# Kernel tuning notes

Measured on AMD Instinct MI355X. Metric: run time of the kernel, lower is better.

## Reference

```python
import jax, jax.numpy as jnp
import numpy as np

B, DZ, L = 1, 128, 256
H, DC = 4, 32
DHC = H * DC


def setup_inputs() -> dict:
    key = jax.random.key(0)
    ks = jax.random.split(key, 6)
    s = 0.02
    return {
        "z": jax.random.normal(ks[0], (B, DZ, L, L), dtype=jnp.float32),
        "ln_w": jnp.ones((DZ,), jnp.float32),
        "ln_b": jnp.zeros((DZ,), jnp.float32),
        "wq": jax.random.normal(ks[1], (DZ, DHC), jnp.float32) * s,
        "bq": jnp.zeros((DHC,), jnp.float32),
        "wk": jax.random.normal(ks[2], (DZ, DHC), jnp.float32) * s,
        "bk": jnp.zeros((DHC,), jnp.float32),
        "wv": jax.random.normal(ks[3], (DZ, DHC), jnp.float32) * s,
        "bv": jnp.zeros((DHC,), jnp.float32),
        "wg": jax.random.normal(ks[4], (DZ, DHC), jnp.float32) * s,
        "bg": jnp.zeros((DHC,), jnp.float32),
        "w2": jax.random.normal(ks[5], (DHC, DZ), jnp.float32) * s,
        "b2": jnp.zeros((DZ,), jnp.float32),
    }


def reference(z, ln_w, ln_b, wq, bq, wk, bk, wv, bv, wg, bg, w2, b2):
    # z: (B, C, L, L) -> (B, n, i, dz)
    zp = jnp.transpose(z, (0, 2, 3, 1))
    # LayerNorm over last dim (torch eps=1e-5)
    mu = jnp.mean(zp, axis=-1, keepdims=True)
    var = jnp.mean(jnp.square(zp - mu), axis=-1, keepdims=True)
    zn = (zp - mu) * jax.lax.rsqrt(var + 1e-5) * ln_w + ln_b

    def proj(w, b):  # (B,n,i,dz) -> (B,n,i,H,DC)
        return (zn @ w + b).reshape(zn.shape[:-1] + (H, DC))

    scalar = jnp.sqrt(jnp.float32(1.0 / DC))
    q = proj(wq, bq)
    k = proj(wk, bk)
    v = proj(wv, bv)
    attn = jnp.einsum('bnihc,bnjhc->bhnij', q * scalar, k)
    attn_w = jax.nn.softmax(attn, axis=-1)
    o = jnp.einsum('bhnij,bnjhc->bnihc', attn_w, v)
    g = jax.nn.sigmoid(zn @ wg + bg).reshape(o.shape)
    zo = (o * g).reshape(o.shape[:-2] + (DHC,))
    out = (zo @ w2 + b2)
    return jnp.transpose(out, (0, 3, 1, 2))  # (B, C, L, L)
```

## Files before the change

### kernel.cpp

```cpp
#include <hip/hip_runtime.h>
#include <cstdint>
#include <cstddef>

#define DZc   128
#define Lc    256
#define Hc    4
#define DCc   32
#define DHCc  128
#define NPOSc (Lc * Lc)

typedef __attribute__((ext_vector_type(8))) short bf16x8;
typedef __attribute__((ext_vector_type(4))) short bf16x4;
typedef __attribute__((ext_vector_type(4))) float f32x4;

static __device__ __forceinline__ unsigned short f2bf(float f) {
  unsigned u = __float_as_uint(f);
  u += 0x7FFFu + ((u >> 16) & 1u);
  return (unsigned short)(u >> 16);
}
static __device__ __forceinline__ float bf2f(unsigned short h) {
  return __uint_as_float(((unsigned)h) << 16);
}
static __device__ __forceinline__ float sigmoidf_(float x) {
  return 1.0f / (1.0f + __expf(-x));
}
static __device__ __forceinline__ unsigned cvtpk(float lo, float hi) {
  unsigned r;
  asm("v_cvt_pk_bf16_f32 %0, %1, %2" : "=v"(r) : "v"(lo), "v"(hi));
  return r;
}

__global__ __launch_bounds__(256) void prep_weights(
    const float* __restrict__ wq, const float* __restrict__ wk,
    const float* __restrict__ wv, const float* __restrict__ wg,
    const float* __restrict__ w2, unsigned short* __restrict__ wT)
{
  const int b = blockIdx.x;
  const int t = threadIdx.x;
  const float* src = (b == 0) ? wq : (b == 1) ? wk : (b == 2) ? wv : (b == 3) ? wg : w2;
  unsigned short* dst = wT + (size_t)b * (DZc * DHCc);
  const float scale = (b == 0) ? 0.17677669529663687f : 1.0f;
  for (int p = 0; p < 64; ++p) {
    const int idx = p * 256 + t;
    const int kk = idx >> 7, j = idx & 127;
    dst[j * 128 + kk] = f2bf(src[idx] * scale);
  }
}

__global__ __launch_bounds__(512, 2) void fused_ln_proj_attn(
    const float* __restrict__ z, const float* __restrict__ lnw, const float* __restrict__ lnb,
    const unsigned short* __restrict__ wT,
    const float* __restrict__ bq, const float* __restrict__ bk,
    const float* __restrict__ bv, const float* __restrict__ bg,
    const float* __restrict__ b2, float* __restrict__ out)
{
  __shared__ unsigned short zkl[Lc * DZc];
  __shared__ unsigned short vtl[DHCc * Lc];
  __shared__ unsigned short pll[8][16 * 64];

  const int t  = threadIdx.x;
  const int n  = blockIdx.x;
  const int w8 = t >> 6;
  const int l  = t & 63;
  const int lr = l & 15;
  const int lg = l >> 4;
  const int h     = w8 & 3;
  const int ihalf = w8 >> 2;

  char* zkb = reinterpret_cast<char*>(zkl);
  char* vtb = reinterpret_cast<char*>(vtl);
  char* plb = reinterpret_cast<char*>(&pll[w8][0]);

  #pragma unroll
  for (int p = 0; p < 2; ++p) {
    const int pq = t >> 4;
    const int cg = t & 15;
    const int gp = n * 256 + p * 128 + pq * 4;
    const int cbase = cg * 8;

    float4 zr[8];
    #pragma unroll
    for (int cc = 0; cc < 8; ++cc)
      zr[cc] = *reinterpret_cast<const float4*>(&z[(size_t)(cbase + cc) * NPOSc + gp]);

    float s[4] = {0.f, 0.f, 0.f, 0.f}, s2[4] = {0.f, 0.f, 0.f, 0.f};
    #pragma unroll
    for (int cc = 0; cc < 8; ++cc) {
      s[0] += zr[cc].x; s2[0] += zr[cc].x * zr[cc].x;
      s[1] += zr[cc].y; s2[1] += zr[cc].y * zr[cc].y;
      s[2] += zr[cc].z; s2[2] += zr[cc].z * zr[cc].z;
      s[3] += zr[cc].w; s2[3] += zr[cc].w * zr[cc].w;
    }
    #pragma unroll
    for (int m = 1; m <= 8; m <<= 1) {
      #pragma unroll
      for (int e = 0; e < 4; ++e) {
        s[e]  += __shfl_xor(s[e],  m);
        s2[e] += __shfl_xor(s2[e], m);
      }
    }
    float mu[4], rs[4];
    #pragma unroll
    for (int e = 0; e < 4; ++e) {
      mu[e] = s[e] * (1.0f / DZc);
      const float var = s2[e] * (1.0f / DZc) - mu[e] * mu[e];
      rs[e] = rsqrtf(var + 1e-5f);
    }
    float lw[8], lb[8];
    #pragma unroll
    for (int q4 = 0; q4 < 2; ++q4) {
      const float4 a = *reinterpret_cast<const float4*>(&lnw[cbase + q4 * 4]);
      const float4 b = *reinterpret_cast<const float4*>(&lnb[cbase + q4 * 4]);
      lw[q4 * 4 + 0] = a.x; lw[q4 * 4 + 1] = a.y; lw[q4 * 4 + 2] = a.z; lw[q4 * 4 + 3] = a.w;
      lb[q4 * 4 + 0] = b.x; lb[q4 * 4 + 1] = b.y; lb[q4 * 4 + 2] = b.z; lb[q4 * 4 + 3] = b.w;
    }
    #pragma unroll
    for (int e = 0; e < 4; ++e) {
      const int i = p * 128 + pq * 4 + e;
      float zn[8];
      #pragma unroll
      for (int cc = 0; cc < 8; ++cc) {
        const float zc = (e == 0) ? zr[cc].x : (e == 1) ? zr[cc].y
                       : (e == 2) ? zr[cc].z : zr[cc].w;
        zn[cc] = (zc - mu[e]) * rs[e] * lw[cc] + lb[cc];
      }
      uint4 pw;
      pw.x = cvtpk(zn[0], zn[1]); pw.y = cvtpk(zn[2], zn[3]);
      pw.z = cvtpk(zn[4], zn[5]); pw.w = cvtpk(zn[6], zn[7]);
      int byte = i * 256 + cbase * 2;
      byte ^= ((i & 15) << 4);
      *reinterpret_cast<uint4*>(zkb + byte) = pw;
    }
  }
  __syncthreads();

  const unsigned short* wqT = wT;
  const unsigned short* wkT = wT + 1 * (DZc * DHCc);
  const unsigned short* wvT = wT + 2 * (DZc * DHCc);
  const unsigned short* wgT = wT + 3 * (DZc * DHCc);

  bf16x8 qfrag[8];
  {
    bf16x8 bfq[2][4];
    float4 qb4[2];
    #pragma unroll
    for (int jt = 0; jt < 2; ++jt) {
      #pragma unroll
      for (int kt = 0; kt < 4; ++kt)
        bfq[jt][kt] = *reinterpret_cast<const bf16x8*>(
            &wqT[(size_t)(h * 32 + jt * 16 + lr) * 128 + kt * 32 + lg * 8]);
      qb4[jt] = *reinterpret_cast<const float4*>(&bq[h * 32 + jt * 16 + lg * 4]);
      qb4[jt].x *= 0.17677669529663687f; qb4[jt].y *= 0.17677669529663687f;
      qb4[jt].z *= 0.17677669529663687f; qb4[jt].w *= 0.17677669529663687f;
    }
    #pragma unroll
    for (int it = 0; it < 8; ++it) {
      bf16x8 af[4];
      #pragma unroll
      for (int kt = 0; kt < 4; ++kt) {
        const int i = ihalf * 128 + it * 16 + lr;
        int byte = i * 256 + (kt * 64 + lg * 16);
        byte ^= ((i & 15) << 4);
        af[kt] = *reinterpret_cast<const bf16x8*>(zkb + byte);
      }
      f32x4 qa[2];
      qa[0] = (f32x4){0.f, 0.f, 0.f, 0.f};
      qa[1] = (f32x4){0.f, 0.f, 0.f, 0.f};
      #pragma unroll
      for (int kt = 0; kt < 4; ++kt)
        #pragma unroll
        for (int jt = 0; jt < 2; ++jt)
          qa[jt] = __builtin_amdgcn_mfma_f32_16x16x32_bf16(bfq[jt][kt], af[kt], qa[jt], 0, 0, 0);
      unsigned srcw0[2], srcw1[2];
      srcw0[0] = cvtpk(qa[0][0] + qb4[0].x, qa[0][1] + qb4[0].y);
      srcw0[1] = cvtpk(qa[0][2] + qb4[0].z, qa[0][3] + qb4[0].w);
      srcw1[0] = cvtpk(qa[1][0] + qb4[1].x, qa[1][1] + qb4[1].y);
      srcw1[1] = cvtpk(qa[1][2] + qb4[1].z, qa[1][3] + qb4[1].w);
      unsigned qw[4];
      #pragma unroll
      for (int i4 = 0; i4 < 4; ++i4) {
        const int quad = lg * 2 + (i4 >> 1);
        const int srcl = (quad & 3) * 16 + lr;
        const unsigned a = (unsigned)__shfl((int)srcw0[i4 & 1], srcl);
        const unsigned b = (unsigned)__shfl((int)srcw1[i4 & 1], srcl);
        qw[i4] = (lg >= 2) ? b : a;
      }
      uint4 qv; qv.x = qw[0]; qv.y = qw[1]; qv.z = qw[2]; qv.w = qw[3];
      qfrag[it] = *reinterpret_cast<const bf16x8*>(&qv);
    }
  }

  unsigned gpk[8][2][2];
  {
    bf16x8 bfg[2][4];
    float gb[2];
    #pragma unroll
    for (int jt = 0; jt < 2; ++jt) {
      #pragma unroll
      for (int kt = 0; kt < 4; ++kt)
        bfg[jt][kt] = *reinterpret_cast<const bf16x8*>(
            &wgT[(size_t)(h * 32 + jt * 16 + lr) * 128 + kt * 32 + lg * 8]);
      gb[jt] = bg[h * 32 + jt * 16 + lr];
    }
    #pragma unroll
    for (int it = 0; it < 8; ++it) {
      bf16x8 af[4];
      #pragma unroll
      for (int kt = 0; kt < 4; ++kt) {
        const int i = ihalf * 128 + it * 16 + lr;
        int byte = i * 256 + (kt * 64 + lg * 16);
        byte ^= ((i & 15) << 4);
        af[kt] = *reinterpret_cast<const bf16x8*>(zkb + byte);
      }
      f32x4 ga[2];
      ga[0] = (f32x4){0.f, 0.f, 0.f, 0.f};
      ga[1] = (f32x4){0.f, 0.f, 0.f, 0.f};
      #pragma unroll
      for (int kt = 0; kt < 4; ++kt)
        #pragma unroll
        for (int jt = 0; jt < 2; ++jt)
          ga[jt] = __builtin_amdgcn_mfma_f32_16x16x32_bf16(af[kt], bfg[jt][kt], ga[jt], 0, 0, 0);
      #pragma unroll
      for (int jt = 0; jt < 2; ++jt) {
        gpk[it][jt][0] = cvtpk(sigmoidf_(ga[jt][0] + gb[jt]), sigmoidf_(ga[jt][1] + gb[jt]));
        gpk[it][jt][1] = cvtpk(sigmoidf_(ga[jt][2] + gb[jt]), sigmoidf_(ga[jt][3] + gb[jt]));
      }
    }
  }

  {
    const int chq = w8 & 3, vih = w8 >> 2;
    bf16x8 bfv[2][4];
    float vb[2];
    #pragma unroll
    for (int jt = 0; jt < 2; ++jt) {
      #pragma unroll
      for (int kt = 0; kt < 4; ++kt)
        bfv[jt][kt] = *reinterpret_cast<const bf16x8*>(
            &wvT[(size_t)(chq * 32 + jt * 16 + lr) * 128 + kt * 32 + lg * 8]);
      vb[jt] = bv[chq * 32 + jt * 16 + lr];
    }
    #pragma unroll 1
    for (int it = 0; it < 8; ++it) {
      bf16x8 af[4];
      #pragma unroll
      for (int kt = 0; kt < 4; ++kt) {
        const int i = vih * 128 + it * 16 + lr;
        int byte = i * 256 + (kt * 64 + lg * 16);
        byte ^= ((i & 15) << 4);
        af[kt] = *reinterpret_cast<const bf16x8*>(zkb + byte);
      }
      f32x4 va[2];
      va[0] = (f32x4){0.f, 0.f, 0.f, 0.f};
      va[1] = (f32x4){0.f, 0.f, 0.f, 0.f};
      #pragma unroll
      for (int kt = 0; kt < 4; ++kt)
        #pragma unroll
        for (int jt = 0; jt < 2; ++jt)
          va[jt] = __builtin_amdgcn_mfma_f32_16x16x32_bf16(af[kt], bfv[jt][kt], va[jt], 0, 0, 0);
      const int ii0 = vih * 128 + it * 16 + lg * 4;
      #pragma unroll
      for (int jt = 0; jt < 2; ++jt) {
        const int ch = chq * 32 + jt * 16 + lr;
        uint2 pv;
        pv.x = cvtpk(va[jt][0] + vb[jt], va[jt][1] + vb[jt]);
        pv.y = cvtpk(va[jt][2] + vb[jt], va[jt][3] + vb[jt]);
        int byte = ch * 512 + ii0 * 2;
        byte ^= ((ch & 7) << 4);
        *reinterpret_cast<uint2*>(vtb + byte) = pv;
      }
    }
  }

  {
    bf16x8 bfk[4];
    #pragma unroll
    for (int kt = 0; kt < 4; ++kt)
      bfk[kt] = *reinterpret_cast<const bf16x8*>(
          &wkT[(size_t)(w8 * 16 + lr) * 128 + kt * 32 + lg * 8]);
    const float4 kb4 = *reinterpret_cast<const float4*>(&bk[w8 * 16 + lg * 4]);
    const float kb[4] = {kb4.x, kb4.y, kb4.z, kb4.w};

    #pragma unroll 1
    for (int c = 0; c < 4; ++c) {
      bf16x8 afr[4][4];
      #pragma unroll
      for (int itc = 0; itc < 4; ++itc)
        #pragma unroll
        for (int kt = 0; kt < 4; ++kt) {
          const int i = c * 64 + itc * 16 + lr;
          int byte = i * 256 + (kt * 64 + lg * 16);
          byte ^= ((i & 15) << 4);
          afr[itc][kt] = *reinterpret_cast<const bf16x8*>(zkb + byte);
        }
      __syncthreads();
      #pragma unroll
      for (int itc = 0; itc < 4; ++itc) {
        f32x4 ka = (f32x4){0.f, 0.f, 0.f, 0.f};
        #pragma unroll
        for (int kt = 0; kt < 4; ++kt)
          ka = __builtin_amdgcn_mfma_f32_16x16x32_bf16(bfk[kt], afr[itc][kt], ka, 0, 0, 0);
        const int j = c * 64 + itc * 16 + lr;
        uint2 pkk;
        pkk.x = cvtpk(ka[0] + kb[0], ka[1] + kb[1]);
        pkk.y = cvtpk(ka[2] + kb[2], ka[3] + kb[3]);
        int byte = j * 256 + (w8 * 16 + lg * 4) * 2;
        byte ^= ((j & 15) << 4);
        *reinterpret_cast<uint2*>(zkb + byte) = pkk;
      }
      __syncthreads();
    }
  }

  unsigned ogpk[8][4];
  #pragma unroll
  for (int it = 0; it < 8; ++it) {
    f32x4 sacc[16];
    #pragma unroll
    for (int jt = 0; jt < 16; ++jt) sacc[jt] = (f32x4){0.f, 0.f, 0.f, 0.f};
    #pragma unroll
    for (int jt = 0; jt < 16; ++jt) {
      const int j = jt * 16 + lr;
      int byte = j * 256 + h * 64 + lg * 16;
      byte ^= ((j & 15) << 4);
      bf16x8 kf = *reinterpret_cast<const bf16x8*>(zkb + byte);
      sacc[jt] = __builtin_amdgcn_mfma_f32_16x16x32_bf16(kf, qfrag[it], sacc[jt], 0, 0, 0);
    }

    float psum = 0.f;
    #pragma unroll
    for (int jt = 0; jt < 16; ++jt)
      #pragma unroll
      for (int r = 0; r < 4; ++r) {
        const float e = __expf(sacc[jt][r]);
        sacc[jt][r] = e;
        psum += e;
      }
    psum += __shfl_xor(psum, 16);
    psum += __shfl_xor(psum, 32);
    const float rl = 1.0f / psum;

    f32x4 oacc[2];
    oacc[0] = (f32x4){0.f, 0.f, 0.f, 0.f};
    oacc[1] = (f32x4){0.f, 0.f, 0.f, 0.f};
    #pragma unroll
    for (int qr = 0; qr < 4; ++qr) {
      #pragma unroll
      for (int jj = 0; jj < 4; ++jj) {
        const int jt = qr * 4 + jj;
        uint2 pk;
        pk.x = cvtpk(sacc[jt][0], sacc[jt][1]);
        pk.y = cvtpk(sacc[jt][2], sacc[jt][3]);
        int byte = lr * 128 + (jj * 16 + lg * 4) * 2;
        byte ^= ((lr & 7) << 4);
        *reinterpret_cast<uint2*>(plb + byte) = pk;
      }
      asm volatile("s_waitcnt lgkmcnt(0)" ::: "memory");
      __builtin_amdgcn_sched_barrier(0);
      #pragma unroll
      for (int kq = 0; kq < 2; ++kq) {
        int pbyte = lr * 128 + (kq * 64 + lg * 16);
        pbyte ^= ((lr & 7) << 4);
        bf16x8 pf = *reinterpret_cast<const bf16x8*>(plb + pbyte);
        #pragma unroll
        for (int cht = 0; cht < 2; ++cht) {
          const int ch = h * 32 + cht * 16 + lr;
          int vbyte = ch * 512 + (qr * 128 + kq * 64 + lg * 16);
          vbyte ^= ((ch & 7) << 4);
          bf16x8 vf = *reinterpret_cast<const bf16x8*>(vtb + vbyte);
          oacc[cht] = __builtin_amdgcn_mfma_f32_16x16x32_bf16(pf, vf, oacc[cht], 0, 0, 0);
        }
      }
    }

    {
      #pragma unroll
      for (int cht = 0; cht < 2; ++cht)
        #pragma unroll
        for (int rp = 0; rp < 2; ++rp) {
          const float g0 = bf2f((unsigned short)(gpk[it][cht][rp] & 0xffffu));
          const float g1 = bf2f((unsigned short)(gpk[it][cht][rp] >> 16));
          ogpk[it][cht * 2 + rp] = cvtpk(oacc[cht][rp * 2 + 0] * rl * g0,
                                         oacc[cht][rp * 2 + 1] * rl * g1);
        }
    }
  }

  __syncthreads();
  #pragma unroll
  for (int it = 0; it < 8; ++it)
    #pragma unroll
    for (int cht = 0; cht < 2; ++cht)
      #pragma unroll
      for (int r = 0; r < 4; ++r) {
        const int pos = ihalf * 128 + it * 16 + lg * 4 + r;
        const int ch  = h * 32 + cht * 16 + lr;
        int byte = pos * 256 + ch * 2;
        byte ^= ((pos & 15) << 4);
        *reinterpret_cast<unsigned short*>(zkb + byte) =
            (unsigned short)(ogpk[it][cht * 2 + (r >> 1)] >> ((r & 1) * 16));
      }
  __syncthreads();

  {
    const unsigned short* w2T = wT + 4 * (DZc * DHCc);
    bf16x8 zb[2][4];
    #pragma unroll
    for (int sub = 0; sub < 2; ++sub) {
      const int pos = w8 * 32 + sub * 16 + lr;
      #pragma unroll
      for (int kt = 0; kt < 4; ++kt) {
        int byte = pos * 256 + kt * 64 + lg * 16;
        byte ^= ((pos & 15) << 4);
        zb[sub][kt] = *reinterpret_cast<const bf16x8*>(zkb + byte);
      }
    }
    #pragma unroll
    for (int ct = 0; ct < 8; ++ct) {
      bf16x8 af[4];
      #pragma unroll
      for (int kt = 0; kt < 4; ++kt)
        af[kt] = *reinterpret_cast<const bf16x8*>(
            &w2T[(size_t)(ct * 16 + lr) * 128 + kt * 32 + lg * 8]);
      #pragma unroll
      for (int sub = 0; sub < 2; ++sub) {
        f32x4 acc = (f32x4){0.f, 0.f, 0.f, 0.f};
        #pragma unroll
        for (int kt = 0; kt < 4; ++kt)
          acc = __builtin_amdgcn_mfma_f32_16x16x32_bf16(af[kt], zb[sub][kt], acc, 0, 0, 0);
        const size_t gpos = (size_t)n * 256 + w8 * 32 + sub * 16 + lr;
        #pragma unroll
        for (int r = 0; r < 4; ++r) {
          const int c = ct * 16 + lg * 4 + r;
          out[(size_t)c * NPOSc + gpos] = acc[r] + b2[c];
        }
      }
    }
  }
}

extern "C" void kernel_launch(void* const* d_in, const int* in_sizes, int n_in,
                              void* d_out, int out_size, void* d_ws, size_t ws_size,
                              hipStream_t stream) {
  const float* z   = (const float*)d_in[0];
  const float* lnw = (const float*)d_in[1];
  const float* lnb = (const float*)d_in[2];
  const float* wq  = (const float*)d_in[3];
  const float* bq  = (const float*)d_in[4];
  const float* wk  = (const float*)d_in[5];
  const float* bk  = (const float*)d_in[6];
  const float* wv  = (const float*)d_in[7];
  const float* bv  = (const float*)d_in[8];
  const float* wg  = (const float*)d_in[9];
  const float* bg  = (const float*)d_in[10];
  const float* w2  = (const float*)d_in[11];
  const float* b2  = (const float*)d_in[12];
  float* out = (float*)d_out;

  unsigned short* wT = (unsigned short*)d_ws;

  prep_weights<<<5, 256, 0, stream>>>(wq, wk, wv, wg, w2, wT);
  fused_ln_proj_attn<<<Lc, 512, 0, stream>>>(
      z, lnw, lnb, wT, bq, bk, bv, bg, b2, out);
}
```

Baseline: 69.72 us.

## Chunk score computation per 64-key block and hoist K projection barriers

The attention loop now computes QK scores, exponentials and P·V for one 64-key chunk at a time, so only 4 score accumulators are live instead of 16. The softmax row sum is reduced after all chunks. The K projection is restructured to compute all 16 tiles into registers first, then write them back to LDS after a single barrier, replacing 8 barriers with 2. This aims to lower register pressure and synchronisation cost, but holds 16 uint2 K results in registers across the projection.

```diff
diff --git a/kernel.cpp b/kernel.cpp
--- a/kernel.cpp
+++ b/kernel.cpp
@@ -272,6 +272,7 @@
     }
   }
 
+  uint2 kreg[16];
   {
     bf16x8 bfk[4];
     #pragma unroll
@@ -281,76 +282,69 @@
     const float4 kb4 = *reinterpret_cast<const float4*>(&bk[w8 * 16 + lg * 4]);
     const float kb[4] = {kb4.x, kb4.y, kb4.z, kb4.w};
 
-    #pragma unroll 1
-    for (int c = 0; c < 4; ++c) {
-      bf16x8 afr[4][4];
-      #pragma unroll
-      for (int itc = 0; itc < 4; ++itc)
-        #pragma unroll
-        for (int kt = 0; kt < 4; ++kt) {
-          const int i = c * 64 + itc * 16 + lr;
-          int byte = i * 256 + (kt * 64 + lg * 16);
-          byte ^= ((i & 15) << 4);
-          afr[itc][kt] = *reinterpret_cast<const bf16x8*>(zkb + byte);
-        }
-      __syncthreads();
-      #pragma unroll
-      for (int itc = 0; itc < 4; ++itc) {
-        f32x4 ka = (f32x4){0.f, 0.f, 0.f, 0.f};
-        #pragma unroll
-        for (int kt = 0; kt < 4; ++kt)
-          ka = __builtin_amdgcn_mfma_f32_16x16x32_bf16(bfk[kt], afr[itc][kt], ka, 0, 0, 0);
-        const int j = c * 64 + itc * 16 + lr;
-        uint2 pkk;
-        pkk.x = cvtpk(ka[0] + kb[0], ka[1] + kb[1]);
-        pkk.y = cvtpk(ka[2] + kb[2], ka[3] + kb[3]);
-        int byte = j * 256 + (w8 * 16 + lg * 4) * 2;
-        byte ^= ((j & 15) << 4);
-        *reinterpret_cast<uint2*>(zkb + byte) = pkk;
-      }
-      __syncthreads();
-    }
-  }
+    #pragma unroll
+    for (int itt = 0; itt < 16; ++itt) {
+      bf16x8 af[4];
+      #pragma unroll
+      for (int kt = 0; kt < 4; ++kt) {
+        const int i = itt * 16 + lr;
+        int byte = i * 256 + (kt * 64 + lg * 16);
+        byte ^= ((i & 15) << 4);
+        af[kt] = *reinterpret_cast<const bf16x8*>(zkb + byte);
+      }
+      f32x4 ka = (f32x4){0.f, 0.f, 0.f, 0.f};
+      #pragma unroll
+      for (int kt = 0; kt < 4; ++kt)
+        ka = __builtin_amdgcn_mfma_f32_16x16x32_bf16(bfk[kt], af[kt], ka, 0, 0, 0);
+      kreg[itt].x = cvtpk(ka[0] + kb[0], ka[1] + kb[1]);
+      kreg[itt].y = cvtpk(ka[2] + kb[2], ka[3] + kb[3]);
+    }
+  }
+  __syncthreads();
+
+  #pragma unroll
+  for (int itt = 0; itt < 16; ++itt) {
+    const int j = itt * 16 + lr;
+    int byte = j * 256 + (w8 * 16 + lg * 4) * 2;
+    byte ^= ((j & 15) << 4);
+    *reinterpret_cast<uint2*>(zkb + byte) = kreg[itt];
+  }
+  __syncthreads();
 
   unsigned ogpk[8][4];
   #pragma unroll
   for (int it = 0; it < 8; ++it) {
-    f32x4 sacc[16];
-    #pragma unroll
-    for (int jt = 0; jt < 16; ++jt) sacc[jt] = (f32x4){0.f, 0.f, 0.f, 0.f};
-    #pragma unroll
-    for (int jt = 0; jt < 16; ++jt) {
-      const int j = jt * 16 + lr;
-      int byte = j * 256 + h * 64 + lg * 16;
-      byte ^= ((j & 15) << 4);
-      bf16x8 kf = *reinterpret_cast<const bf16x8*>(zkb + byte);
-      sacc[jt] = __builtin_amdgcn_mfma_f32_16x16x32_bf16(kf, qfrag[it], sacc[jt], 0, 0, 0);
-    }
-
     float psum = 0.f;
-    #pragma unroll
-    for (int jt = 0; jt < 16; ++jt)
-      #pragma unroll
-      for (int r = 0; r < 4; ++r) {
-        const float e = __expf(sacc[jt][r]);
-        sacc[jt][r] = e;
-        psum += e;
-      }
-    psum += __shfl_xor(psum, 16);
-    psum += __shfl_xor(psum, 32);
-    const float rl = 1.0f / psum;
-
     f32x4 oacc[2];
     oacc[0] = (f32x4){0.f, 0.f, 0.f, 0.f};
     oacc[1] = (f32x4){0.f, 0.f, 0.f, 0.f};
+
     #pragma unroll
     for (int qr = 0; qr < 4; ++qr) {
+      f32x4 sacc[4];
+      #pragma unroll
+      for (int jj = 0; jj < 4; ++jj) sacc[jj] = (f32x4){0.f, 0.f, 0.f, 0.f};
       #pragma unroll
       for (int jj = 0; jj < 4; ++jj) {
-        const int jt = qr * 4 + jj;
+        const int j = (qr * 4 + jj) * 16 + lr;
+        int byte = j * 256 + h * 64 + lg * 16;
+        byte ^= ((j & 15) << 4);
+        bf16x8 kf = *reinterpret_cast<const bf16x8*>(zkb + byte);
+        sacc[jj] = __builtin_amdgcn_mfma_f32_16x16x32_bf16(kf, qfrag[it], sacc[jj], 0, 0, 0);
+      }
+      #pragma unroll
+      for (int jj = 0; jj < 4; ++jj)
+        #pragma unroll
+        for (int r = 0; r < 4; ++r) {
+          const float e = __expf(sacc[jj][r]);
+          sacc[jj][r] = e;
+          psum += e;
+        }
+      #pragma unroll
+      for (int jj = 0; jj < 4; ++jj) {
         uint2 pk;
-        pk.x = cvtpk(sacc[jt][0], sacc[jt][1]);
-        pk.y = cvtpk(sacc[jt][2], sacc[jt][3]);
+        pk.x = cvtpk(sacc[jj][0], sacc[jj][1]);
+        pk.y = cvtpk(sacc[jj][2], sacc[jj][3]);
         int byte = lr * 128 + (jj * 16 + lg * 4) * 2;
         byte ^= ((lr & 7) << 4);
         *reinterpret_cast<uint2*>(plb + byte) = pk;
@@ -373,17 +367,19 @@
       }
     }
 
-    {
-      #pragma unroll
-      for (int cht = 0; cht < 2; ++cht)
-        #pragma unroll
-        for (int rp = 0; rp < 2; ++rp) {
-          const float g0 = bf2f((unsigned short)(gpk[it][cht][rp] & 0xffffu));
-          const float g1 = bf2f((unsigned short)(gpk[it][cht][rp] >> 16));
-          ogpk[it][cht * 2 + rp] = cvtpk(oacc[cht][rp * 2 + 0] * rl * g0,
-                                         oacc[cht][rp * 2 + 1] * rl * g1);
-        }
-    }
+    psum += __shfl_xor(psum, 16);
+    psum += __shfl_xor(psum, 32);
+    const float rl = 1.0f / psum;
+
+    #pragma unroll
+    for (int cht = 0; cht < 2; ++cht)
+      #pragma unroll
+      for (int rp = 0; rp < 2; ++rp) {
+        const float g0 = bf2f((unsigned short)(gpk[it][cht][rp] & 0xffffu));
+        const float g1 = bf2f((unsigned short)(gpk[it][cht][rp] >> 16));
+        ogpk[it][cht * 2 + rp] = cvtpk(oacc[cht][rp * 2 + 0] * rl * g0,
+                                       oacc[cht][rp * 2 + 1] * rl * g1);
+      }
   }
 
   __syncthreads();
```

After: 67.79 us (median of 2 runs). -2.8%, faster.
